# Kernel tuning notes

Hardware: AMD Instinct MI355X
Metric: run time of the kernel (lower is better)

## Reference

```python
import jax, jax.numpy as jnp
import numpy as np

HID = 1024       # hidden_size
H = 8            # num_attention_heads
KVH = 2          # num_key_value_heads
D = HID // H     # head_dim = 128
WINDOW = 2048    # sliding_window
THETA = 10000.0  # rope_theta
B, S = 1, 4096


def rotate_half(x):
    x1, x2 = jnp.split(x, 2, axis=-1)
    return jnp.concatenate([-x2, x1], axis=-1)


def setup_inputs() -> dict:
    key = jax.random.key(0)
    ks = jax.random.split(key, 5)
    scale = 0.02
    return {
        "hidden_states": jax.random.normal(ks[0], (B, S, HID), dtype=jnp.float32),
        "wq": jax.random.normal(ks[1], (H * D, HID), dtype=jnp.float32) * scale,
        "wk": jax.random.normal(ks[2], (KVH * D, HID), dtype=jnp.float32) * scale,
        "wv": jax.random.normal(ks[3], (KVH * D, HID), dtype=jnp.float32) * scale,
        "wo": jax.random.normal(ks[4], (HID, H * D), dtype=jnp.float32) * scale,
        "position_ids": jnp.broadcast_to(jnp.arange(S, dtype=jnp.int64 if jax.config.jax_enable_x64 else jnp.int32)[None, :], (B, S)),
    }


def reference(hidden_states, wq, wk, wv, wo, position_ids):
    b, s, _ = hidden_states.shape
    # projections (torch nn.Linear: x @ W^T)
    q = (hidden_states @ wq.T).reshape(b, s, H, D).transpose(0, 2, 1, 3)      # bhsd
    k = (hidden_states @ wk.T).reshape(b, s, KVH, D).transpose(0, 2, 1, 3)    # b(kv)sd
    v = (hidden_states @ wv.T).reshape(b, s, KVH, D).transpose(0, 2, 1, 3)

    # RoPE cache (head_dim, seq_len)
    inv_freq = 1.0 / THETA ** (jnp.arange(0, D, 2, dtype=jnp.float32) / D)
    t = jnp.arange(s, dtype=jnp.float32)
    freqs = t[:, None] * inv_freq[None, :]
    emb = jnp.concatenate([freqs, freqs], axis=-1)           # (S, D)
    cos = jnp.cos(emb)[position_ids][:, None]                # (B,1,S,D)
    sin = jnp.sin(emb)[position_ids][:, None]
    q = q * cos + rotate_half(q) * sin
    k = k * cos + rotate_half(k) * sin

    # GQA: repeat kv heads to match query heads (repeat_interleave on head dim)
    groups = H // KVH
    k = jnp.repeat(k, groups, axis=1)
    v = jnp.repeat(v, groups, axis=1)

    # full score matrix with sliding-window causal mask
    scores = jnp.einsum("bhqd,bhkd->bhqk", q, k)
    i = jnp.arange(s)[:, None]
    j = jnp.arange(s)[None, :]
    mask = (j <= i) & (j > i - WINDOW)                       # causal + window
    scores = jnp.where(mask[None, None], scores, -jnp.inf) / jnp.sqrt(jnp.float32(D))

    probs = jax.nn.softmax(scores.astype(jnp.float32), axis=-1).astype(q.dtype)
    ctx = jnp.einsum("bhqk,bhkd->bhqd", probs, v)
    ctx = ctx.transpose(0, 2, 1, 3).reshape(b, s, H * D)
    return ctx @ wo.T
```

## Files before the change

kernel.cpp:

```cpp
#include <hip/hip_runtime.h>

#define S_LEN 4096
#define HIDDEN 1024
#define NH 8
#define NKV 2
#define HD 128
#define WIN 2048

typedef short bf16x8 __attribute__((ext_vector_type(8)));
typedef float f32x4 __attribute__((ext_vector_type(4)));
typedef unsigned short u16x4 __attribute__((ext_vector_type(4)));

__device__ __forceinline__ unsigned short f2b(float f) {
    unsigned int u = __builtin_bit_cast(unsigned int, f);
    u += 0x7fffu + ((u >> 16) & 1u);
    return (unsigned short)(u >> 16);
}
__device__ __forceinline__ float b2f(unsigned short u) {
    unsigned int x = ((unsigned int)u) << 16;
    return __builtin_bit_cast(float, x);
}

__device__ __forceinline__ void gl_lds16(const unsigned short* g, unsigned short* l) {
    __builtin_amdgcn_global_load_lds(
        (const __attribute__((address_space(1))) unsigned int*)g,
        (__attribute__((address_space(3))) unsigned int*)l, 16, 0, 0);
}

#define WAIT_VM8   0x0F78
#define WAIT_VM0   0x0F70
#define WAIT_LGKM0 0xC07F

__global__ __launch_bounds__(256) void cvt5(
    const float* __restrict__ s0, unsigned short* __restrict__ t0, int n0,
    const float* __restrict__ s1, unsigned short* __restrict__ t1, int n1,
    const float* __restrict__ s2, unsigned short* __restrict__ t2, int n2,
    const float* __restrict__ s3, unsigned short* __restrict__ t3, int n3,
    const float* __restrict__ s4, unsigned short* __restrict__ t4, int n4)
{
    int i = blockIdx.x * 256 + threadIdx.x;
    const float* s; unsigned short* t;
    if (i < n0)              { s = s0; t = t0; }
    else if ((i -= n0) < n1) { s = s1; t = t1; }
    else if ((i -= n1) < n2) { s = s2; t = t2; }
    else if ((i -= n2) < n3) { s = s3; t = t3; }
    else if ((i -= n3) < n4) { s = s4; t = t4; }
    else return;
    f32x4 v = *(const f32x4*)(s + (size_t)i * 4);
    u16x4 r = { f2b(v[0]), f2b(v[1]), f2b(v[2]), f2b(v[3]) };
    *(u16x4*)(t + (size_t)i * 4) = r;
}

__global__ __launch_bounds__(256, 2) void gemm128(
    const unsigned short* __restrict__ A, const unsigned short* __restrict__ W,
    float* __restrict__ Cf, unsigned short* __restrict__ Cb,
    int M, int N, int K)
{
    __shared__ alignas(16) unsigned short As[128 * 32];
    __shared__ alignas(16) unsigned short Bs[128 * 32];

    int lane = threadIdx.x & 63;
    int w = threadIdx.x >> 6;
    int l15 = lane & 15, quad = lane >> 4;

    int tiles_n = N >> 7;
    int mt0 = (int)blockIdx.x / tiles_n;
    int nt0 = (int)blockIdx.x - mt0 * tiles_n;

    size_t goffA[2], goffB[2];
    #pragma unroll
    for (int is = 0; is < 2; ++is) {
        int s = w * 128 + is * 64 + lane;
        int row = s >> 2, spos = s & 3;
        int kblk = spos ^ ((row >> 1) & 3);
        goffA[is] = (size_t)(mt0 * 128 + row) * K + kblk * 8;
        goffB[is] = (size_t)(nt0 * 128 + row) * K + kblk * 8;
    }
    unsigned short* dstA0 = As + (w * 128 + 0) * 8;
    unsigned short* dstA1 = As + (w * 128 + 64) * 8;
    unsigned short* dstB0 = Bs + (w * 128 + 0) * 8;
    unsigned short* dstB1 = Bs + (w * 128 + 64) * 8;

    int arow0 = (w >> 1) * 64;
    int brow0 = (w & 1) * 64;
    int aoff[4], boff[4];
    #pragma unroll
    for (int t = 0; t < 4; ++t) {
        int ra = arow0 + t * 16 + l15;
        aoff[t] = (ra * 4 + (quad ^ ((ra >> 1) & 3))) * 8;
        int rb = brow0 + t * 16 + l15;
        boff[t] = (rb * 4 + (quad ^ ((rb >> 1) & 3))) * 8;
    }

    f32x4 acc[4][4];
    #pragma unroll
    for (int i = 0; i < 4; ++i)
        #pragma unroll
        for (int j = 0; j < 4; ++j) acc[i][j] = (f32x4){0.f, 0.f, 0.f, 0.f};

    for (int k0 = 0; k0 < K; k0 += 32) {
        gl_lds16(A + goffA[0] + k0, dstA0);
        gl_lds16(A + goffA[1] + k0, dstA1);
        gl_lds16(W + goffB[0] + k0, dstB0);
        gl_lds16(W + goffB[1] + k0, dstB1);
        __syncthreads();

        bf16x8 af[4], bf_[4];
        #pragma unroll
        for (int t = 0; t < 4; ++t) {
            af[t]  = *(const bf16x8*)(As + aoff[t]);
            bf_[t] = *(const bf16x8*)(Bs + boff[t]);
        }
        #pragma unroll
        for (int i = 0; i < 4; ++i)
            #pragma unroll
            for (int j = 0; j < 4; ++j)
                acc[i][j] = __builtin_amdgcn_mfma_f32_16x16x32_bf16(af[i], bf_[j], acc[i][j], 0, 0, 0);
        __syncthreads();
    }

    #pragma unroll
    for (int i = 0; i < 4; ++i) {
        int row0 = mt0 * 128 + arow0 + i * 16 + quad * 4;
        #pragma unroll
        for (int j = 0; j < 4; ++j) {
            int col = nt0 * 128 + brow0 + j * 16 + l15;
            if (Cf) {
                #pragma unroll
                for (int reg = 0; reg < 4; ++reg)
                    Cf[(size_t)(row0 + reg) * N + col] = acc[i][j][reg];
            } else {
                #pragma unroll
                for (int reg = 0; reg < 4; ++reg)
                    Cb[(size_t)(row0 + reg) * N + col] = f2b(acc[i][j][reg]);
            }
        }
    }
}

#define QKVW (HIDDEN + 2 * NKV * HD)
__global__ __launch_bounds__(256, 2) void gemmqkv(
    const unsigned short* __restrict__ A, const unsigned short* __restrict__ W,
    const int* __restrict__ pos,
    unsigned short* __restrict__ Qb, unsigned short* __restrict__ Kb,
    unsigned short* __restrict__ Vg)
{
    __shared__ alignas(16) unsigned short As[128 * 32];
    __shared__ alignas(16) unsigned short Bs[128 * 32];
    __shared__ float Ex[4][32][68];

    int lane = threadIdx.x & 63;
    int w = threadIdx.x >> 6;
    int l15 = lane & 15, quad = lane >> 4;

    const int K = HIDDEN;
    int mt0 = (int)blockIdx.x / 12;
    int nt0 = (int)blockIdx.x - mt0 * 12;

    size_t goffA[2], goffB[2];
    #pragma unroll
    for (int is = 0; is < 2; ++is) {
        int s = w * 128 + is * 64 + lane;
        int row = s >> 2, spos = s & 3;
        int kblk = spos ^ ((row >> 1) & 3);
        goffA[is] = (size_t)(mt0 * 128 + row) * K + kblk * 8;
        goffB[is] = (size_t)(nt0 * 128 + row) * K + kblk * 8;
    }
    unsigned short* dstA0 = As + (w * 128 + 0) * 8;
    unsigned short* dstA1 = As + (w * 128 + 64) * 8;
    unsigned short* dstB0 = Bs + (w * 128 + 0) * 8;
    unsigned short* dstB1 = Bs + (w * 128 + 64) * 8;

    int arow0 = (w >> 1) * 64;
    int brow0 = (w & 1) * 64;
    int aoff[4], boff[4];
    #pragma unroll
    for (int t = 0; t < 4; ++t) {
        int ra = arow0 + t * 16 + l15;
        aoff[t] = (ra * 4 + (quad ^ ((ra >> 1) & 3))) * 8;
        int rb = brow0 + t * 16 + l15;
        boff[t] = (rb * 4 + (quad ^ ((rb >> 1) & 3))) * 8;
    }

    f32x4 acc[4][4];
    #pragma unroll
    for (int i = 0; i < 4; ++i)
        #pragma unroll
        for (int j = 0; j < 4; ++j) acc[i][j] = (f32x4){0.f, 0.f, 0.f, 0.f};

    for (int k0 = 0; k0 < K; k0 += 32) {
        gl_lds16(A + goffA[0] + k0, dstA0);
        gl_lds16(A + goffA[1] + k0, dstA1);
        gl_lds16(W + goffB[0] + k0, dstB0);
        gl_lds16(W + goffB[1] + k0, dstB1);
        __syncthreads();

        bf16x8 af[4], bf_[4];
        #pragma unroll
        for (int t = 0; t < 4; ++t) {
            af[t]  = *(const bf16x8*)(As + aoff[t]);
            bf_[t] = *(const bf16x8*)(Bs + boff[t]);
        }
        #pragma unroll
        for (int i = 0; i < 4; ++i)
            #pragma unroll
            for (int j = 0; j < 4; ++j)
                acc[i][j] = __builtin_amdgcn_mfma_f32_16x16x32_bf16(af[i], bf_[j], acc[i][j], 0, 0, 0);
        __syncthreads();
    }

    if (nt0 >= 10) {
        int kv = nt0 - 10;
        #pragma unroll
        for (int i = 0; i < 4; ++i) {
            int row0 = mt0 * 128 + arow0 + i * 16 + quad * 4;
            #pragma unroll
            for (int j = 0; j < 4; ++j) {
                int col = kv * 128 + brow0 + j * 16 + l15;
                #pragma unroll
                for (int reg = 0; reg < 4; ++reg)
                    Vg[(size_t)(row0 + reg) * (NKV * HD) + col] = f2b(acc[i][j][reg]);
            }
        }
        return;
    }

    bool isQ = (nt0 < 8);
    int kv = nt0 - 8;
    bool is64 = (pos[1] == 0) && (pos[3] == 0);
    const float qscale = 0.08838834764831843f;

    float invf[4];
    #pragma unroll
    for (int j = 0; j < 4; ++j) {
        int d6 = (brow0 + j * 16 + l15) & 63;
        invf[j] = exp2f(-(float)d6 * (13.287712379549449f / 64.0f));
    }

    #pragma unroll
    for (int r2 = 0; r2 < 2; ++r2) {
        #pragma unroll
        for (int ii = 0; ii < 2; ++ii) {
            int i = r2 * 2 + ii;
            #pragma unroll
            for (int j = 0; j < 4; ++j)
                #pragma unroll
                for (int reg = 0; reg < 4; ++reg)
                    Ex[w][ii * 16 + quad * 4 + reg][j * 16 + l15] = acc[i][j][reg];
        }
        __syncthreads();
        #pragma unroll
        for (int ii = 0; ii < 2; ++ii) {
            int i = r2 * 2 + ii;
            #pragma unroll
            for (int reg = 0; reg < 4; ++reg) {
                int s = mt0 * 128 + arow0 + i * 16 + quad * 4 + reg;
                int pv_ = is64 ? pos[2 * s] : pos[s];
                float pf = (float)pv_;
                #pragma unroll
                for (int j = 0; j < 4; ++j) {
                    float sn, cs;
                    __sincosf(pf * invf[j], &sn, &cs);
                    float a  = acc[i][j][reg];
                    float pr = Ex[w ^ 1][ii * 16 + quad * 4 + reg][j * 16 + l15];
                    int d_local = brow0 + j * 16 + l15;
                    float outv = (d_local < 64) ? (a * cs - pr * sn) : (a * cs + pr * sn);
                    if (isQ) {
                        Qb[(size_t)s * HIDDEN + nt0 * HD + d_local] = f2b(outv * qscale);
                    } else {
                        Kb[(size_t)kv * S_LEN * HD + (size_t)s * HD + d_local] = f2b(outv);
                    }
                }
            }
        }
        __syncthreads();
    }
}

__global__ __launch_bounds__(256) void vtrans(
    const unsigned short* __restrict__ Vg, unsigned short* __restrict__ Vt)
{
    __shared__ unsigned short L[64][66];
    int st = (int)blockIdx.x >> 2, dt = (int)blockIdx.x & 3;
    int s0 = st * 64, d0 = dt * 64;
    int tid = threadIdx.x;
    {
        int dl = tid & 63, sl4 = tid >> 6;
        #pragma unroll
        for (int p = 0; p < 16; ++p) {
            int sl = p * 4 + sl4;
            L[sl][dl] = Vg[(size_t)(s0 + sl) * (NKV * HD) + d0 + dl];
        }
    }
    __syncthreads();
    {
        int sl = tid & 63, dl4 = tid >> 6;
        #pragma unroll
        for (int p = 0; p < 16; ++p) {
            int dl = p * 4 + dl4;
            Vt[(size_t)(d0 + dl) * S_LEN + s0 + sl] = L[sl][dl];
        }
    }
}

__global__ __launch_bounds__(256, 2) void attn_coop(
    const unsigned short* __restrict__ Qb, const unsigned short* __restrict__ Kb,
    const unsigned short* __restrict__ Vt, unsigned short* __restrict__ Ctx)
{
    __shared__ alignas(16) unsigned short Klds[2][64 * 128];
    __shared__ alignas(16) unsigned short Vlds[2][128 * 64];
    __shared__ alignas(16) unsigned short Plds[4][16 * 72];

    int lane = threadIdx.x & 63;
    int w = threadIdx.x >> 6;
    int l15 = lane & 15, quad = lane >> 4;
    int h = blockIdx.y;
    int kv = h >> 2;
    int qb = blockIdx.x * 64;
    int q16 = qb + w * 16;

    bf16x8 a_q[4];
    const unsigned short* qrow = Qb + (size_t)(q16 + l15) * HIDDEN + h * HD + quad * 8;
    #pragma unroll
    for (int st = 0; st < 4; ++st) a_q[st] = *(const bf16x8*)(qrow + st * 32);

    bf16x8 b_one;
    #pragma unroll
    for (int i = 0; i < 8; ++i) b_one[i] = (short)0x3F80;

    int lo = qb + 63 - (WIN - 1); if (lo < 0) lo = 0; lo &= ~63;
    int nch = (qb + 64 - lo) >> 6;

    const unsigned short* gbase;
    unsigned short* ldsdst[2];
    int myoff[8];
    int jmul;
    if (w < 2) {
        gbase = Kb + (size_t)kv * S_LEN * HD;
        ldsdst[0] = &Klds[0][w * 8 * 512];
        ldsdst[1] = &Klds[1][w * 8 * 512];
        jmul = HD;
        #pragma unroll
        for (int tt = 0; tt < 8; ++tt) {
            int t = w * 8 + tt;
            int key  = t * 4 + (lane >> 4);
            int dblk = (lane & 15) ^ (key & 15);
            myoff[tt] = key * HD + dblk * 8;
        }
    } else {
        gbase = Vt + (size_t)kv * HD * S_LEN;
        ldsdst[0] = &Vlds[0][(w - 2) * 8 * 512];
        ldsdst[1] = &Vlds[1][(w - 2) * 8 * 512];
        jmul = 1;
        #pragma unroll
        for (int tt = 0; tt < 8; ++tt) {
            int t = (w - 2) * 8 + tt;
            int d    = t * 8 + (lane >> 3);
            int kblk = (lane & 7) ^ (d & 7);
            myoff[tt] = d * S_LEN + kblk * 8;
        }
    }

    auto issue = [&](int c) {
        int j0 = lo + c * 64;
        const unsigned short* src = gbase + (size_t)j0 * jmul;
        unsigned short* dst = ldsdst[c & 1];
        #pragma unroll
        for (int tt = 0; tt < 8; ++tt)
            gl_lds16(src + myoff[tt], dst + tt * 512);
    };

    f32x4 o[9];
    #pragma unroll
    for (int nd = 0; nd < 9; ++nd) o[nd] = (f32x4){0.f, 0.f, 0.f, 0.f};

    unsigned short* pw = &Plds[w][0];

    auto do_scores = [&](int c, const unsigned short* Kc) {
        int j0 = lo + c * 64;
        f32x4 sc[4];
        #pragma unroll
        for (int t = 0; t < 4; ++t) {
            sc[t] = (f32x4){0.f, 0.f, 0.f, 0.f};
            int key = t * 16 + l15;
            #pragma unroll
            for (int st = 0; st < 4; ++st) {
                int off16 = key * 16 + ((st * 4 + quad) ^ (key & 15));
                bf16x8 bk = *(const bf16x8*)(Kc + off16 * 8);
                sc[t] = __builtin_amdgcn_mfma_f32_16x16x32_bf16(a_q[st], bk, sc[t], 0, 0, 0);
            }
        }
        float p[4][4];
        if (j0 + 63 <= q16 && j0 > q16 + 15 - WIN) {
            #pragma unroll
            for (int t = 0; t < 4; ++t)
                #pragma unroll
                for (int reg = 0; reg < 4; ++reg) p[t][reg] = __expf(sc[t][reg]);
        } else {
            #pragma unroll
            for (int t = 0; t < 4; ++t) {
                int jj = j0 + t * 16 + l15;
                #pragma unroll
                for (int reg = 0; reg < 4; ++reg) {
                    int i = q16 + quad * 4 + reg;
                    p[t][reg] = (jj <= i && jj > i - WIN) ? __expf(sc[t][reg]) : 0.f;
                }
            }
        }
        #pragma unroll
        for (int t = 0; t < 4; ++t)
            #pragma unroll
            for (int reg = 0; reg < 4; ++reg)
                pw[(quad * 4 + reg) * 72 + t * 16 + l15] = f2b(p[t][reg]);
    };

    auto do_pv = [&](int cm1) {
        bf16x8 a_p0 = *(const bf16x8*)(pw + l15 * 72 + quad * 8);
        bf16x8 a_p1 = *(const bf16x8*)(pw + l15 * 72 + 32 + quad * 8);
        const unsigned short* Vc = &Vlds[cm1 & 1][0];
        #pragma unroll
        for (int nd = 0; nd < 8; ++nd) {
            int d = nd * 16 + l15;
            int o16a = d * 8 + ((quad) ^ (d & 7));
            int o16b = d * 8 + ((4 + quad) ^ (d & 7));
            bf16x8 bv0 = *(const bf16x8*)(Vc + o16a * 8);
            bf16x8 bv1 = *(const bf16x8*)(Vc + o16b * 8);
            o[nd] = __builtin_amdgcn_mfma_f32_16x16x32_bf16(a_p0, bv0, o[nd], 0, 0, 0);
            o[nd] = __builtin_amdgcn_mfma_f32_16x16x32_bf16(a_p1, bv1, o[nd], 0, 0, 0);
        }
        o[8] = __builtin_amdgcn_mfma_f32_16x16x32_bf16(a_p0, b_one, o[8], 0, 0, 0);
        o[8] = __builtin_amdgcn_mfma_f32_16x16x32_bf16(a_p1, b_one, o[8], 0, 0, 0);
    };

    if (w < 2) issue(0);

    {
        if (1 < nch) {
            if (w < 2) issue(1); else issue(0);
            __asm__ volatile("" ::: "memory");
            __builtin_amdgcn_s_waitcnt(WAIT_VM8);
        } else {
            if (w >= 2) issue(0);
            __asm__ volatile("" ::: "memory");
            __builtin_amdgcn_s_waitcnt(WAIT_VM0);
        }
        __builtin_amdgcn_s_barrier();
        __asm__ volatile("" ::: "memory");
        do_scores(0, &Klds[0][0]);
        __builtin_amdgcn_s_waitcnt(WAIT_LGKM0);
        __builtin_amdgcn_s_barrier();
        __asm__ volatile("" ::: "memory");
    }

    for (int c = 1; c < nch; ++c) {
        if (c + 1 < nch) {
            if (w < 2) issue(c + 1); else issue(c);
            __asm__ volatile("" ::: "memory");
            __builtin_amdgcn_s_waitcnt(WAIT_VM8);
        } else {
            if (w >= 2) issue(c);
            __asm__ volatile("" ::: "memory");
            __builtin_amdgcn_s_waitcnt(WAIT_VM0);
        }
        __builtin_amdgcn_s_barrier();
        __asm__ volatile("" ::: "memory");

        do_pv(c - 1);
        do_scores(c, &Klds[c & 1][0]);

        __asm__ volatile("" ::: "memory");
        __builtin_amdgcn_s_waitcnt(WAIT_LGKM0);
        __builtin_amdgcn_s_barrier();
        __asm__ volatile("" ::: "memory");
    }

    do_pv(nch - 1);

    #pragma unroll
    for (int nd = 0; nd < 8; ++nd) {
        int d = nd * 16 + l15;
        #pragma unroll
        for (int reg = 0; reg < 4; ++reg) {
            int q = q16 + quad * 4 + reg;
            Ctx[(size_t)q * HIDDEN + h * HD + d] = f2b(o[nd][reg] / o[8][reg]);
        }
    }
}

extern "C" void kernel_launch(void* const* d_in, const int* in_sizes, int n_in,
                              void* d_out, int out_size, void* d_ws, size_t ws_size,
                              hipStream_t stream)
{
    const float* hidden = (const float*)d_in[0];
    const float* wq = (const float*)d_in[1];
    const float* wk = (const float*)d_in[2];
    const float* wv = (const float*)d_in[3];
    const float* wo = (const float*)d_in[4];
    const int* pos = (const int*)d_in[5];
    float* out = (float*)d_out;

    char* ws = (char*)d_ws;
    size_t off = 0;
    unsigned short* Hb   = (unsigned short*)(ws + off); off += (size_t)S_LEN * HIDDEN * 2;
    unsigned short* Wqkv = (unsigned short*)(ws + off); off += (size_t)QKVW * HIDDEN * 2;
    unsigned short* Wob  = (unsigned short*)(ws + off); off += (size_t)HIDDEN * HIDDEN * 2;
    unsigned short* Qb   = (unsigned short*)(ws + off); off += (size_t)S_LEN * HIDDEN * 2;
    unsigned short* Kb   = (unsigned short*)(ws + off); off += (size_t)S_LEN * NKV * HD * 2;
    unsigned short* Vg   = (unsigned short*)(ws + off); off += (size_t)S_LEN * NKV * HD * 2;
    unsigned short* Vt   = (unsigned short*)(ws + off); off += (size_t)S_LEN * NKV * HD * 2;
    unsigned short* Cb   = (unsigned short*)(ws + off); off += (size_t)S_LEN * HIDDEN * 2;

    const int n_h  = S_LEN * HIDDEN / 4;
    const int n_wq = HIDDEN * HIDDEN / 4;
    const int n_wk = NKV * HD * HIDDEN / 4;
    int tot4 = n_h + n_wq + 2 * n_wk + n_wq;
    cvt5<<<(tot4 + 255) / 256, 256, 0, stream>>>(
        hidden, Hb, n_h,
        wq, Wqkv, n_wq,
        wk, Wqkv + (size_t)HIDDEN * HIDDEN, n_wk,
        wv, Wqkv + (size_t)(HIDDEN + NKV * HD) * HIDDEN, n_wk,
        wo, Wob, n_wq);

    gemmqkv<<<(S_LEN / 128) * 12, 256, 0, stream>>>(
        Hb, Wqkv, pos, Qb, Kb, Vg);

    vtrans<<<(S_LEN / 64) * ((NKV * HD) / 64), 256, 0, stream>>>(Vg, Vt);

    attn_coop<<<dim3(S_LEN / 64, NH), 256, 0, stream>>>(Qb, Kb, Vt, Cb);

    gemm128<<<(S_LEN / 128) * (HIDDEN / 128), 256, 0, stream>>>(
        Cb, Wob, out, nullptr, S_LEN, HIDDEN, HIDDEN);
}
```

Baseline: 194.2 us.

## Double-buffer GEMM LDS tiles and shrink attention chunks to raise occupancy

Both projection GEMMs now use double-buffered LDS tiles, so the next K-slice is prefetched with global_load_lds while MFMAs run on the current slice. The per-iteration __syncthreads pair is replaced by explicit waitcnt/barrier. The attention kernel drops from 64-key to 32-key chunks with every wave loading K and V, removes the skewed PV-of-previous-chunk pipeline, and swizzles the P staging buffer. With halved LDS it requests 4 blocks per CU instead of 2. This trades more barriers and shorter MFMA bursts per chunk for more latency hiding through occupancy and prefetch.

```diff
diff --git a/kernel.cpp b/kernel.cpp
--- a/kernel.cpp
+++ b/kernel.cpp
@@ -27,9 +27,10 @@
         (__attribute__((address_space(3))) unsigned int*)l, 16, 0, 0);
 }
 
-#define WAIT_VM8   0x0F78
+#define WAIT_VM4   0x0F74
 #define WAIT_VM0   0x0F70
 #define WAIT_LGKM0 0xC07F
+#define MEMFENCE() __asm__ volatile("" ::: "memory")
 
 __global__ __launch_bounds__(256) void cvt5(
     const float* __restrict__ s0, unsigned short* __restrict__ t0, int n0,
@@ -56,8 +57,8 @@
     float* __restrict__ Cf, unsigned short* __restrict__ Cb,
     int M, int N, int K)
 {
-    __shared__ alignas(16) unsigned short As[128 * 32];
-    __shared__ alignas(16) unsigned short Bs[128 * 32];
+    __shared__ alignas(16) unsigned short As[2][128 * 32];
+    __shared__ alignas(16) unsigned short Bs[2][128 * 32];
 
     int lane = threadIdx.x & 63;
     int w = threadIdx.x >> 6;
@@ -76,10 +77,6 @@
         goffA[is] = (size_t)(mt0 * 128 + row) * K + kblk * 8;
         goffB[is] = (size_t)(nt0 * 128 + row) * K + kblk * 8;
     }
-    unsigned short* dstA0 = As + (w * 128 + 0) * 8;
-    unsigned short* dstA1 = As + (w * 128 + 64) * 8;
-    unsigned short* dstB0 = Bs + (w * 128 + 0) * 8;
-    unsigned short* dstB1 = Bs + (w * 128 + 64) * 8;
 
     int arow0 = (w >> 1) * 64;
     int brow0 = (w & 1) * 64;
@@ -98,25 +95,46 @@
         #pragma unroll
         for (int j = 0; j < 4; ++j) acc[i][j] = (f32x4){0.f, 0.f, 0.f, 0.f};
 
-    for (int k0 = 0; k0 < K; k0 += 32) {
-        gl_lds16(A + goffA[0] + k0, dstA0);
-        gl_lds16(A + goffA[1] + k0, dstA1);
-        gl_lds16(W + goffB[0] + k0, dstB0);
-        gl_lds16(W + goffB[1] + k0, dstB1);
-        __syncthreads();
-
+    auto stage = [&](int i) {
+        int b = i & 1, k0 = i * 32;
+        gl_lds16(A + goffA[0] + k0, &As[b][(w * 128 + 0) * 8]);
+        gl_lds16(A + goffA[1] + k0, &As[b][(w * 128 + 64) * 8]);
+        gl_lds16(W + goffB[0] + k0, &Bs[b][(w * 128 + 0) * 8]);
+        gl_lds16(W + goffB[1] + k0, &Bs[b][(w * 128 + 64) * 8]);
+    };
+
+    int nk = K >> 5;
+    stage(0);
+    for (int i = 0; i < nk; ++i) {
+        if (i + 1 < nk) {
+            stage(i + 1);
+            MEMFENCE();
+            __builtin_amdgcn_s_waitcnt(WAIT_VM4);
+        } else {
+            MEMFENCE();
+            __builtin_amdgcn_s_waitcnt(WAIT_VM0);
+        }
+        __builtin_amdgcn_s_barrier();
+        MEMFENCE();
+
+        const unsigned short* Ab = &As[i & 1][0];
+        const unsigned short* Bb = &Bs[i & 1][0];
         bf16x8 af[4], bf_[4];
         #pragma unroll
         for (int t = 0; t < 4; ++t) {
-            af[t]  = *(const bf16x8*)(As + aoff[t]);
-            bf_[t] = *(const bf16x8*)(Bs + boff[t]);
-        }
-        #pragma unroll
-        for (int i = 0; i < 4; ++i)
+            af[t]  = *(const bf16x8*)(Ab + aoff[t]);
+            bf_[t] = *(const bf16x8*)(Bb + boff[t]);
+        }
+        #pragma unroll
+        for (int i2 = 0; i2 < 4; ++i2)
             #pragma unroll
             for (int j = 0; j < 4; ++j)
-                acc[i][j] = __builtin_amdgcn_mfma_f32_16x16x32_bf16(af[i], bf_[j], acc[i][j], 0, 0, 0);
-        __syncthreads();
+                acc[i2][j] = __builtin_amdgcn_mfma_f32_16x16x32_bf16(af[i2], bf_[j], acc[i2][j], 0, 0, 0);
+
+        MEMFENCE();
+        __builtin_amdgcn_s_waitcnt(WAIT_LGKM0);
+        __builtin_amdgcn_s_barrier();
+        MEMFENCE();
     }
 
     #pragma unroll
@@ -145,8 +163,8 @@
     unsigned short* __restrict__ Qb, unsigned short* __restrict__ Kb,
     unsigned short* __restrict__ Vg)
 {
-    __shared__ alignas(16) unsigned short As[128 * 32];
-    __shared__ alignas(16) unsigned short Bs[128 * 32];
+    __shared__ alignas(16) unsigned short As[2][128 * 32];
+    __shared__ alignas(16) unsigned short Bs[2][128 * 32];
     __shared__ float Ex[4][32][68];
 
     int lane = threadIdx.x & 63;
@@ -166,10 +184,6 @@
         goffA[is] = (size_t)(mt0 * 128 + row) * K + kblk * 8;
         goffB[is] = (size_t)(nt0 * 128 + row) * K + kblk * 8;
     }
-    unsigned short* dstA0 = As + (w * 128 + 0) * 8;
-    unsigned short* dstA1 = As + (w * 128 + 64) * 8;
-    unsigned short* dstB0 = Bs + (w * 128 + 0) * 8;
-    unsigned short* dstB1 = Bs + (w * 128 + 64) * 8;
 
     int arow0 = (w >> 1) * 64;
     int brow0 = (w & 1) * 64;
@@ -188,25 +202,45 @@
         #pragma unroll
         for (int j = 0; j < 4; ++j) acc[i][j] = (f32x4){0.f, 0.f, 0.f, 0.f};
 
-    for (int k0 = 0; k0 < K; k0 += 32) {
-        gl_lds16(A + goffA[0] + k0, dstA0);
-        gl_lds16(A + goffA[1] + k0, dstA1);
-        gl_lds16(W + goffB[0] + k0, dstB0);
-        gl_lds16(W + goffB[1] + k0, dstB1);
-        __syncthreads();
-
+    auto stage = [&](int i) {
+        int b = i & 1, k0 = i * 32;
+        gl_lds16(A + goffA[0] + k0, &As[b][(w * 128 + 0) * 8]);
+        gl_lds16(A + goffA[1] + k0, &As[b][(w * 128 + 64) * 8]);
+        gl_lds16(W + goffB[0] + k0, &Bs[b][(w * 128 + 0) * 8]);
+        gl_lds16(W + goffB[1] + k0, &Bs[b][(w * 128 + 64) * 8]);
+    };
+
+    stage(0);
+    for (int i = 0; i < 32; ++i) {
+        if (i + 1 < 32) {
+            stage(i + 1);
+            MEMFENCE();
+            __builtin_amdgcn_s_waitcnt(WAIT_VM4);
+        } else {
+            MEMFENCE();
+            __builtin_amdgcn_s_waitcnt(WAIT_VM0);
+        }
+        __builtin_amdgcn_s_barrier();
+        MEMFENCE();
+
+        const unsigned short* Ab = &As[i & 1][0];
+        const unsigned short* Bb = &Bs[i & 1][0];
         bf16x8 af[4], bf_[4];
         #pragma unroll
         for (int t = 0; t < 4; ++t) {
-            af[t]  = *(const bf16x8*)(As + aoff[t]);
-            bf_[t] = *(const bf16x8*)(Bs + boff[t]);
-        }
-        #pragma unroll
-        for (int i = 0; i < 4; ++i)
+            af[t]  = *(const bf16x8*)(Ab + aoff[t]);
+            bf_[t] = *(const bf16x8*)(Bb + boff[t]);
+        }
+        #pragma unroll
+        for (int i2 = 0; i2 < 4; ++i2)
             #pragma unroll
             for (int j = 0; j < 4; ++j)
-                acc[i][j] = __builtin_amdgcn_mfma_f32_16x16x32_bf16(af[i], bf_[j], acc[i][j], 0, 0, 0);
-        __syncthreads();
+                acc[i2][j] = __builtin_amdgcn_mfma_f32_16x16x32_bf16(af[i2], bf_[j], acc[i2][j], 0, 0, 0);
+
+        MEMFENCE();
+        __builtin_amdgcn_s_waitcnt(WAIT_LGKM0);
+        __builtin_amdgcn_s_barrier();
+        MEMFENCE();
     }
 
     if (nt0 >= 10) {
@@ -303,13 +337,13 @@
     }
 }
 
-__global__ __launch_bounds__(256, 2) void attn_coop(
+__global__ __launch_bounds__(256, 4) void attn_coop(
     const unsigned short* __restrict__ Qb, const unsigned short* __restrict__ Kb,
     const unsigned short* __restrict__ Vt, unsigned short* __restrict__ Ctx)
 {
-    __shared__ alignas(16) unsigned short Klds[2][64 * 128];
-    __shared__ alignas(16) unsigned short Vlds[2][128 * 64];
-    __shared__ alignas(16) unsigned short Plds[4][16 * 72];
+    __shared__ alignas(16) unsigned short Klds[2][32 * 128];
+    __shared__ alignas(16) unsigned short Vlds[2][128 * 32];
+    __shared__ alignas(16) unsigned short Plds[4][512];
 
     int lane = threadIdx.x & 63;
     int w = threadIdx.x >> 6;
@@ -328,46 +362,34 @@
     #pragma unroll
     for (int i = 0; i < 8; ++i) b_one[i] = (short)0x3F80;
 
-    int lo = qb + 63 - (WIN - 1); if (lo < 0) lo = 0; lo &= ~63;
-    int nch = (qb + 64 - lo) >> 6;
-
-    const unsigned short* gbase;
-    unsigned short* ldsdst[2];
-    int myoff[8];
-    int jmul;
-    if (w < 2) {
-        gbase = Kb + (size_t)kv * S_LEN * HD;
-        ldsdst[0] = &Klds[0][w * 8 * 512];
-        ldsdst[1] = &Klds[1][w * 8 * 512];
-        jmul = HD;
-        #pragma unroll
-        for (int tt = 0; tt < 8; ++tt) {
-            int t = w * 8 + tt;
-            int key  = t * 4 + (lane >> 4);
-            int dblk = (lane & 15) ^ (key & 15);
-            myoff[tt] = key * HD + dblk * 8;
-        }
-    } else {
-        gbase = Vt + (size_t)kv * HD * S_LEN;
-        ldsdst[0] = &Vlds[0][(w - 2) * 8 * 512];
-        ldsdst[1] = &Vlds[1][(w - 2) * 8 * 512];
-        jmul = 1;
-        #pragma unroll
-        for (int tt = 0; tt < 8; ++tt) {
-            int t = (w - 2) * 8 + tt;
-            int d    = t * 8 + (lane >> 3);
-            int kblk = (lane & 7) ^ (d & 7);
-            myoff[tt] = d * S_LEN + kblk * 8;
-        }
+    int lo = qb + 63 - (WIN - 1); if (lo < 0) lo = 0; lo &= ~31;
+    int nch = (qb + 64 - lo) >> 5;
+
+    const unsigned short* kbaseG = Kb + (size_t)kv * S_LEN * HD;
+    const unsigned short* vbaseG = Vt + (size_t)kv * HD * S_LEN;
+    int offK[2], dstK[2], offV[2], dstV[2];
+    #pragma unroll
+    for (int tt = 0; tt < 2; ++tt) {
+        int t = w * 2 + tt;
+        int key  = t * 4 + (lane >> 4);
+        int dblk = (lane & 15) ^ (key & 15);
+        offK[tt] = key * HD + dblk * 8;
+        dstK[tt] = t * 512;
+        int d    = t * 16 + (lane >> 2);
+        int kblk = (lane & 3) ^ (d & 3);
+        offV[tt] = d * S_LEN + kblk * 8;
+        dstV[tt] = t * 512;
     }
 
     auto issue = [&](int c) {
-        int j0 = lo + c * 64;
-        const unsigned short* src = gbase + (size_t)j0 * jmul;
-        unsigned short* dst = ldsdst[c & 1];
-        #pragma unroll
-        for (int tt = 0; tt < 8; ++tt)
-            gl_lds16(src + myoff[tt], dst + tt * 512);
+        int j0 = lo + c * 32;
+        int b = c & 1;
+        const unsigned short* ks = kbaseG + (size_t)j0 * HD;
+        const unsigned short* vs = vbaseG + j0;
+        gl_lds16(ks + offK[0], &Klds[b][dstK[0]]);
+        gl_lds16(ks + offK[1], &Klds[b][dstK[1]]);
+        gl_lds16(vs + offV[0], &Vlds[b][dstV[0]]);
+        gl_lds16(vs + offV[1], &Vlds[b][dstV[1]]);
     };
 
     f32x4 o[9];
@@ -376,11 +398,38 @@
 
     unsigned short* pw = &Plds[w][0];
 
-    auto do_scores = [&](int c, const unsigned short* Kc) {
-        int j0 = lo + c * 64;
-        f32x4 sc[4];
-        #pragma unroll
-        for (int t = 0; t < 4; ++t) {
+    int pwr[2][4];
+    #pragma unroll
+    for (int t = 0; t < 2; ++t)
+        #pragma unroll
+        for (int reg = 0; reg < 4; ++reg) {
+            int row = quad * 4 + reg;
+            int slot = row * 4 + (((t * 2) + (l15 >> 3)) ^ (row & 3));
+            pwr[t][reg] = slot * 8 + (l15 & 7);
+        }
+    int prd = (l15 * 4 + (quad ^ (l15 & 3))) * 8;
+
+    issue(0);
+
+    for (int c = 0; c < nch; ++c) {
+        int j0 = lo + c * 32;
+        if (c + 1 < nch) {
+            issue(c + 1);
+            MEMFENCE();
+            __builtin_amdgcn_s_waitcnt(WAIT_VM4);
+        } else {
+            MEMFENCE();
+            __builtin_amdgcn_s_waitcnt(WAIT_VM0);
+        }
+        __builtin_amdgcn_s_barrier();
+        MEMFENCE();
+
+        const unsigned short* Kc = &Klds[c & 1][0];
+        const unsigned short* Vc = &Vlds[c & 1][0];
+
+        f32x4 sc[2];
+        #pragma unroll
+        for (int t = 0; t < 2; ++t) {
             sc[t] = (f32x4){0.f, 0.f, 0.f, 0.f};
             int key = t * 16 + l15;
             #pragma unroll
@@ -390,15 +439,16 @@
                 sc[t] = __builtin_amdgcn_mfma_f32_16x16x32_bf16(a_q[st], bk, sc[t], 0, 0, 0);
             }
         }
-        float p[4][4];
-        if (j0 + 63 <= q16 && j0 > q16 + 15 - WIN) {
-            #pragma unroll
-            for (int t = 0; t < 4; ++t)
+
+        float p[2][4];
+        if (j0 + 31 <= q16 && j0 > q16 + 15 - WIN) {
+            #pragma unroll
+            for (int t = 0; t < 2; ++t)
                 #pragma unroll
                 for (int reg = 0; reg < 4; ++reg) p[t][reg] = __expf(sc[t][reg]);
         } else {
             #pragma unroll
-            for (int t = 0; t < 4; ++t) {
+            for (int t = 0; t < 2; ++t) {
                 int jj = j0 + t * 16 + l15;
                 #pragma unroll
                 for (int reg = 0; reg < 4; ++reg) {
@@ -407,74 +457,33 @@
                 }
             }
         }
-        #pragma unroll
-        for (int t = 0; t < 4; ++t)
+
+        #pragma unroll
+        for (int t = 0; t < 2; ++t)
             #pragma unroll
             for (int reg = 0; reg < 4; ++reg)
-                pw[(quad * 4 + reg) * 72 + t * 16 + l15] = f2b(p[t][reg]);
-    };
-
-    auto do_pv = [&](int cm1) {
-        bf16x8 a_p0 = *(const bf16x8*)(pw + l15 * 72 + quad * 8);
-        bf16x8 a_p1 = *(const bf16x8*)(pw + l15 * 72 + 32 + quad * 8);
-        const unsigned short* Vc = &Vlds[cm1 & 1][0];
+                pw[pwr[t][reg]] = f2b(p[t][reg]);
+
+        __builtin_amdgcn_wave_barrier();
+        __builtin_amdgcn_s_waitcnt(WAIT_LGKM0);
+        __builtin_amdgcn_wave_barrier();
+
+        bf16x8 a_p = *(const bf16x8*)(pw + prd);
+
         #pragma unroll
         for (int nd = 0; nd < 8; ++nd) {
             int d = nd * 16 + l15;
-            int o16a = d * 8 + ((quad) ^ (d & 7));
-            int o16b = d * 8 + ((4 + quad) ^ (d & 7));
-            bf16x8 bv0 = *(const bf16x8*)(Vc + o16a * 8);
-            bf16x8 bv1 = *(const bf16x8*)(Vc + o16b * 8);
-            o[nd] = __builtin_amdgcn_mfma_f32_16x16x32_bf16(a_p0, bv0, o[nd], 0, 0, 0);
-            o[nd] = __builtin_amdgcn_mfma_f32_16x16x32_bf16(a_p1, bv1, o[nd], 0, 0, 0);
-        }
-        o[8] = __builtin_amdgcn_mfma_f32_16x16x32_bf16(a_p0, b_one, o[8], 0, 0, 0);
-        o[8] = __builtin_amdgcn_mfma_f32_16x16x32_bf16(a_p1, b_one, o[8], 0, 0, 0);
-    };
-
-    if (w < 2) issue(0);
-
-    {
-        if (1 < nch) {
-            if (w < 2) issue(1); else issue(0);
-            __asm__ volatile("" ::: "memory");
-            __builtin_amdgcn_s_waitcnt(WAIT_VM8);
-        } else {
-            if (w >= 2) issue(0);
-            __asm__ volatile("" ::: "memory");
-            __builtin_amdgcn_s_waitcnt(WAIT_VM0);
-        }
-        __builtin_amdgcn_s_barrier();
-        __asm__ volatile("" ::: "memory");
-        do_scores(0, &Klds[0][0]);
+            int o16 = d * 4 + (quad ^ (d & 3));
+            bf16x8 bv = *(const bf16x8*)(Vc + o16 * 8);
+            o[nd] = __builtin_amdgcn_mfma_f32_16x16x32_bf16(a_p, bv, o[nd], 0, 0, 0);
+        }
+        o[8] = __builtin_amdgcn_mfma_f32_16x16x32_bf16(a_p, b_one, o[8], 0, 0, 0);
+
+        MEMFENCE();
         __builtin_amdgcn_s_waitcnt(WAIT_LGKM0);
         __builtin_amdgcn_s_barrier();
-        __asm__ volatile("" ::: "memory");
-    }
-
-    for (int c = 1; c < nch; ++c) {
-        if (c + 1 < nch) {
-            if (w < 2) issue(c + 1); else issue(c);
-            __asm__ volatile("" ::: "memory");
-            __builtin_amdgcn_s_waitcnt(WAIT_VM8);
-        } else {
-            if (w >= 2) issue(c);
-            __asm__ volatile("" ::: "memory");
-            __builtin_amdgcn_s_waitcnt(WAIT_VM0);
-        }
-        __builtin_amdgcn_s_barrier();
-        __asm__ volatile("" ::: "memory");
-
-        do_pv(c - 1);
-        do_scores(c, &Klds[c & 1][0]);
-
-        __asm__ volatile("" ::: "memory");
-        __builtin_amdgcn_s_waitcnt(WAIT_LGKM0);
-        __builtin_amdgcn_s_barrier();
-        __asm__ volatile("" ::: "memory");
-    }
-
-    do_pv(nch - 1);
+        MEMFENCE();
+    }
 
     #pragma unroll
     for (int nd = 0; nd < 8; ++nd) {
```

Result: slower. 209.9 us (+8.1%).
